# Kernel tuning notes

Hardware: AMD Instinct MI355X
Metric: run time of the kernel (lower is better)

## Reference

```python
import jax, jax.numpy as jnp
import numpy as np

D_MODEL, D_K, D_V, N_HEADS = 1024, 64, 64, 16
BATCH, N_CTX = 2, 2048


def half_causal_allowed(n):
    # rows [0, n/2): attend to cols [0, n/2) only (dense block)
    # rows [n/2, n): standard causal (col <= row)
    i = jnp.arange(n)[:, None]
    j = jnp.arange(n)[None, :]
    top = (i < n // 2) & (j < n // 2)
    bot = (i >= n // 2) & (j <= i)
    return top | bot  # [n, n] bool


def setup_inputs() -> dict:
    key = jax.random.key(0)
    ks = jax.random.split(key, 8)
    s_in = 1.0 / np.sqrt(D_MODEL)
    s_out = 1.0 / np.sqrt(D_V * N_HEADS)
    return {
        "x": jax.random.normal(ks[0], (BATCH, N_CTX, D_MODEL), jnp.float32),
        # Linear weights stored [in, out] (transpose of torch layout)
        "Wq": jax.random.uniform(ks[1], (D_MODEL, D_K * N_HEADS), jnp.float32, -s_in, s_in),
        "bq": jax.random.uniform(ks[2], (D_K * N_HEADS,), jnp.float32, -s_in, s_in),
        "Wk": jax.random.uniform(ks[3], (D_MODEL, D_K * N_HEADS), jnp.float32, -s_in, s_in),
        "bk": jax.random.uniform(ks[4], (D_K * N_HEADS,), jnp.float32, -s_in, s_in),
        "Wv": jax.random.uniform(ks[5], (D_MODEL, D_V * N_HEADS), jnp.float32, -s_in, s_in),
        "bv": jax.random.uniform(ks[6], (D_V * N_HEADS,), jnp.float32, -s_in, s_in),
        "Wo": jax.random.uniform(ks[7], (D_V * N_HEADS, D_MODEL), jnp.float32, -s_out, s_out),
    }


def reference(x, Wq, bq, Wk, bk, Wv, bv, Wo):
    b, n, _ = x.shape
    h, dk, dv = N_HEADS, D_K, D_V
    # projections -> [b, h, n, d]
    q = (x @ Wq + bq).reshape(b, n, h, dk).transpose(0, 2, 1, 3)
    k = (x @ Wk + bk).reshape(b, n, h, dk).transpose(0, 2, 1, 3)
    v = (x @ Wv + bv).reshape(b, n, h, dv).transpose(0, 2, 1, 3)
    scores = jnp.einsum("bhqd,bhkd->bhqk", q / jnp.sqrt(jnp.float32(dk)), k)
    allowed = half_causal_allowed(n)  # [n, n]
    scores = jnp.where(allowed, scores, -jnp.inf)
    attn = jax.nn.softmax(scores, axis=-1)  # dropout p=0 -> identity
    out = jnp.einsum("bhqk,bhkd->bhqd", attn, v)
    out = out.transpose(0, 2, 1, 3).reshape(b, n, h * dv)
    return out @ Wo  # final Linear has no bias
```

## Files before the change

kernel.cpp:

```cpp
#include <hip/hip_runtime.h>
#include <hip/hip_bf16.h>

#define NH 16
#define DH 64
#define DM 1024
#define NC 2048
#define MROWS 4096
#define KVT 64

#define SCALE_Q 0.180336880f

typedef __attribute__((ext_vector_type(8))) short short8;
typedef __attribute__((ext_vector_type(4))) float f32x4;
typedef __attribute__((ext_vector_type(16))) float f32x16;
typedef __attribute__((ext_vector_type(4))) unsigned int uint4e;

__device__ __forceinline__ unsigned pkbf16(float a, float b) {
    unsigned r;
    asm("v_cvt_pk_bf16_f32 %0, %1, %2" : "=v"(r) : "v"(a), "v"(b));
    return r;
}
__device__ __forceinline__ unsigned short f2bf(float x) {
    return (unsigned short)(pkbf16(x, x) & 0xffffu);
}
__device__ __forceinline__ float exp2v(float x) {
    float r;
    asm("v_exp_f32 %0, %1" : "=v"(r) : "v"(x));
    return r;
}
__device__ __forceinline__ f32x16 fzero16() {
    f32x16 r;
    #pragma unroll
    for (int i = 0; i < 16; ++i) r[i] = 0.f;
    return r;
}
__device__ __forceinline__ short8 mk8(unsigned w0, unsigned w1, unsigned w2, unsigned w3) {
    uint4e u = {w0, w1, w2, w3};
    return __builtin_bit_cast(short8, u);
}
__device__ __forceinline__ void gload16(const unsigned short* g, unsigned short* l) {
    __builtin_amdgcn_global_load_lds(
        (const __attribute__((address_space(1))) void*)g,
        (__attribute__((address_space(3))) void*)l, 16, 0, 0);
}

__global__ __launch_bounds__(256) void prep(const float* __restrict__ x,
                                            const float* __restrict__ W0,
                                            const float* __restrict__ W1,
                                            const float* __restrict__ W2,
                                            const float* __restrict__ W3,
                                            unsigned short* __restrict__ xb,
                                            unsigned short* __restrict__ Wt4)
{
    __shared__ unsigned short T[64][72];
    const int bid = blockIdx.x;
    const int t = threadIdx.x;
    if (bid < 1024) {
        #pragma unroll
        for (int g = 0; g < 2; ++g) {
            const int i = bid * 512 + g * 256 + t;
            const float4 a = ((const float4*)x)[i * 2];
            const float4 b = ((const float4*)x)[i * 2 + 1];
            uint4e u = {pkbf16(a.x, a.y), pkbf16(a.z, a.w),
                        pkbf16(b.x, b.y), pkbf16(b.z, b.w)};
            ((uint4e*)xb)[i] = u;
        }
        return;
    }
    const int z = (bid - 1024) >> 8;
    const int tile = (bid - 1024) & 255;
    const int bi = tile >> 4, bj = tile & 15;
    const float* W = (z == 0) ? W0 : (z == 1) ? W1 : (z == 2) ? W2 : W3;
    unsigned short* Wt = Wt4 + (size_t)z * DM * DM;
    const int r = t >> 2, s = t & 3;
    const float* src = W + (size_t)(bi * 64 + r) * DM + bj * 64 + s * 16;
    float4 f0 = ((const float4*)src)[0];
    float4 f1 = ((const float4*)src)[1];
    float4 f2 = ((const float4*)src)[2];
    float4 f3 = ((const float4*)src)[3];
    uint2 u;
    u.x = pkbf16(f0.x, f0.y); u.y = pkbf16(f0.z, f0.w); *(uint2*)&T[r][s * 16]      = u;
    u.x = pkbf16(f1.x, f1.y); u.y = pkbf16(f1.z, f1.w); *(uint2*)&T[r][s * 16 + 4]  = u;
    u.x = pkbf16(f2.x, f2.y); u.y = pkbf16(f2.z, f2.w); *(uint2*)&T[r][s * 16 + 8]  = u;
    u.x = pkbf16(f3.x, f3.y); u.y = pkbf16(f3.z, f3.w); *(uint2*)&T[r][s * 16 + 12] = u;
    __syncthreads();
    unsigned short vals[16];
    #pragma unroll
    for (int j = 0; j < 16; ++j) vals[j] = T[s * 16 + j][r];
    unsigned short* dst = Wt + (size_t)(bj * 64 + r) * DM + bi * 64 + s * 16;
    *(short8*)(dst)     = *(short8*)&vals[0];
    *(short8*)(dst + 8) = *(short8*)&vals[8];
}

__global__ __launch_bounds__(256) void gemm_qkv(const unsigned short* __restrict__ A,
                                                const unsigned short* __restrict__ Bt,
                                                const float* __restrict__ bq,
                                                const float* __restrict__ bk,
                                                const float* __restrict__ bv,
                                                unsigned short* __restrict__ Out)
{
    __shared__ unsigned short As[128 * 32];
    __shared__ unsigned short Bs[128 * 32];
    const int t  = threadIdx.x;
    const int w  = t >> 6, l = t & 63;
    const int wr = w >> 1, wc = w & 1;
    const int m0 = blockIdx.y << 7;
    const int n0 = blockIdx.x << 7;

    f32x4 acc[4][4] = {};
    const int nkt = DM >> 5;
    for (int kt = 0; kt < nkt; ++kt) {
        #pragma unroll
        for (int j = 0; j < 2; ++j) {
            const int c0 = j * 256 + w * 64;
            const int cc = c0 + l;
            const int row = cc >> 2, qq = cc & 3;
            gload16(A  + (size_t)(m0 + row) * DM + kt * 32 + qq * 8, &As[c0 * 8]);
            gload16(Bt + (size_t)(n0 + row) * DM + kt * 32 + qq * 8, &Bs[c0 * 8]);
        }
        __syncthreads();
        short8 af[4], bf_[4];
        #pragma unroll
        for (int mi = 0; mi < 4; ++mi)
            af[mi] = *(short8*)&As[(wr * 64 + mi * 16 + (l & 15)) * 32 + (l >> 4) * 8];
        #pragma unroll
        for (int ni = 0; ni < 4; ++ni)
            bf_[ni] = *(short8*)&Bs[(wc * 64 + ni * 16 + (l & 15)) * 32 + (l >> 4) * 8];
        #pragma unroll
        for (int mi = 0; mi < 4; ++mi)
            #pragma unroll
            for (int ni = 0; ni < 4; ++ni)
                acc[mi][ni] = __builtin_amdgcn_mfma_f32_16x16x32_bf16(
                                  af[mi], bf_[ni], acc[mi][ni], 0, 0, 0);
        __syncthreads();
    }

    const int seg = n0 >> 10;
    const float* bias = (seg == 0) ? bq : (seg == 1) ? bk : bv;
    const float scale = (seg == 0) ? SCALE_Q : 1.0f;
    const int ncol0 = (n0 & 1023) + wc * 64;
    float bvv[4];
    #pragma unroll
    for (int ni = 0; ni < 4; ++ni)
        bvv[ni] = bias[ncol0 + ni * 16 + (l & 15)];

    if (seg == 2) {
        unsigned short* vt = Out + 2 * (size_t)MROWS * DM;
        #pragma unroll
        for (int mi = 0; mi < 4; ++mi)
            #pragma unroll
            for (int ni = 0; ni < 4; ++ni) {
                const int gcol = ncol0 + ni * 16 + (l & 15);
                const int h_ = gcol >> 6, d_ = gcol & 63;
                #pragma unroll
                for (int r = 0; r < 4; ++r) {
                    const int grow = m0 + wr * 64 + mi * 16 + (l >> 4) * 4 + r;
                    const int b_ = grow >> 11, n_ = grow & 2047;
                    vt[(((size_t)b_ * 16 + h_) * 64 + d_) * NC + n_] =
                        f2bf(acc[mi][ni][r] + bvv[ni]);
                }
            }
    } else {
        unsigned short* C = Out + (size_t)seg * MROWS * DM;
        #pragma unroll
        for (int mi = 0; mi < 4; ++mi)
            #pragma unroll
            for (int ni = 0; ni < 4; ++ni) {
                const int gcol = ncol0 + ni * 16 + (l & 15);
                #pragma unroll
                for (int r = 0; r < 4; ++r) {
                    const int grow = m0 + wr * 64 + mi * 16 + (l >> 4) * 4 + r;
                    C[(size_t)grow * DM + gcol] = f2bf((acc[mi][ni][r] + bvv[ni]) * scale);
                }
            }
    }
}

__global__ __launch_bounds__(256) void gemm_wo(const unsigned short* __restrict__ A,
                                               const unsigned short* __restrict__ Bt,
                                               float* __restrict__ C)
{
    __shared__ unsigned short As[64 * 32];
    __shared__ unsigned short Bs[128 * 32];
    const int t = threadIdx.x, w = t >> 6, l = t & 63;
    const int wr = w >> 1, wc = w & 1;
    const int m0 = blockIdx.y << 6;
    const int n0 = blockIdx.x << 7;

    f32x4 acc[2][4] = {};
    const int nkt = DM >> 5;
    for (int kt = 0; kt < nkt; ++kt) {
        {
            const int c0 = w * 64;
            const int cc = c0 + l;
            const int row = cc >> 2, qq = cc & 3;
            gload16(A + (size_t)(m0 + row) * DM + kt * 32 + qq * 8, &As[c0 * 8]);
        }
        #pragma unroll
        for (int j = 0; j < 2; ++j) {
            const int c0 = j * 256 + w * 64;
            const int cc = c0 + l;
            const int row = cc >> 2, qq = cc & 3;
            gload16(Bt + (size_t)(n0 + row) * DM + kt * 32 + qq * 8, &Bs[c0 * 8]);
        }
        __syncthreads();
        short8 af[2], bf_[4];
        #pragma unroll
        for (int mi = 0; mi < 2; ++mi)
            af[mi] = *(short8*)&As[(wr * 32 + mi * 16 + (l & 15)) * 32 + (l >> 4) * 8];
        #pragma unroll
        for (int ni = 0; ni < 4; ++ni)
            bf_[ni] = *(short8*)&Bs[(wc * 64 + ni * 16 + (l & 15)) * 32 + (l >> 4) * 8];
        #pragma unroll
        for (int mi = 0; mi < 2; ++mi)
            #pragma unroll
            for (int ni = 0; ni < 4; ++ni)
                acc[mi][ni] = __builtin_amdgcn_mfma_f32_16x16x32_bf16(
                                  af[mi], bf_[ni], acc[mi][ni], 0, 0, 0);
        __syncthreads();
    }
    #pragma unroll
    for (int mi = 0; mi < 2; ++mi)
        #pragma unroll
        for (int ni = 0; ni < 4; ++ni) {
            const int gcol = n0 + wc * 64 + ni * 16 + (l & 15);
            #pragma unroll
            for (int r = 0; r < 4; ++r) {
                const int grow = m0 + wr * 32 + mi * 16 + (l >> 4) * 4 + r;
                C[(size_t)grow * DM + gcol] = acc[mi][ni][r];
            }
        }
}

__global__ __launch_bounds__(128, 2) void attn_nosm(const unsigned short* __restrict__ Qg,
                                                    const unsigned short* __restrict__ Kg,
                                                    const unsigned short* __restrict__ Vtg,
                                                    unsigned short* __restrict__ Og)
{
    __shared__ unsigned short KS[2][4096];
    __shared__ unsigned short VS[2][4096];
    const int t   = threadIdx.x;
    const int w   = t >> 6;
    const int l   = t & 63;
    const int l31 = l & 31;
    const int hi  = l >> 5;

    const int f   = blockIdx.x;
    const int xcd = f & 7;
    const int pos = f >> 3;
    const int bh  = xcd * 4 + (pos >> 5);
    int qt = pos & 31;
    if ((pos >> 5) & 1) qt = 31 - qt;
    const int b = bh >> 4;
    const int h = bh & 15;

    const int qb = qt << 6;
    const int wq = qb + w * 32;
    const size_t rb0 = (size_t)b * NC;
    const int hd = h * DH;

    const unsigned short* qp = Qg + (rb0 + wq + l31) * DM + hd + hi * 8;
    short8 fq[4];
    #pragma unroll
    for (int c = 0; c < 4; ++c)
        fq[c] = *(const short8*)(qp + c * 16);

    f32x16 o0 = fzero16(), o1 = fzero16();
    f32x16 lacc = fzero16();
    const bool bottom = (qb >= NC / 2);
    const int nkv = bottom ? (qt + 1) : 16;

    const unsigned short* Vbase = Vtg + (size_t)bh * 64 * NC;

    auto stage = [&](int it, int buf) {
        const int kb = it * KVT;
        #pragma unroll
        for (int j = 0; j < 4; ++j) {
            const int jj  = w * 4 + j;
            const int p   = jj * 64 + l;
            const int row = p >> 3;
            const int slot = (p & 7) ^ (row & 7);
            gload16(Kg + (size_t)(rb0 + kb + row) * DM + hd + slot * 8,
                    &KS[buf][jj * 512]);
            gload16(Vbase + (size_t)row * NC + kb + slot * 8,
                    &VS[buf][jj * 512]);
        }
    };

    stage(0, 0);
    if (nkv > 1) stage(1, 1);

    for (int it = 0; it < nkv; ++it) {
        const int kb = it * KVT;
        const int cur = it & 1;
        if (it + 1 < nkv) {
            asm volatile("s_waitcnt vmcnt(8)" ::: "memory");
        } else {
            asm volatile("s_waitcnt vmcnt(0)" ::: "memory");
        }
        __builtin_amdgcn_s_barrier();

        short8 kf[2][4], vf[2][4];
        #pragma unroll
        for (int half = 0; half < 2; ++half) {
            const int row = half * 32 + l31;
            const int rx  = row & 7;
            #pragma unroll
            for (int c = 0; c < 4; ++c) {
                const int slot = (c * 2 + hi) ^ rx;
                kf[half][c] = *(const short8*)(&KS[cur][row * 64 + slot * 8]);
                vf[half][c] = *(const short8*)(&VS[cur][row * 64 + slot * 8]);
            }
        }
        asm volatile("s_waitcnt lgkmcnt(0)" ::: "memory");
        __builtin_amdgcn_sched_barrier(0);
        __builtin_amdgcn_s_barrier();

        if (it + 2 < nkv) stage(it + 2, cur);

        const bool active = bottom ? (kb <= wq + 31) : true;
        if (active) {
            f32x16 s0 = fzero16(), s1 = fzero16();
            __builtin_amdgcn_s_setprio(1);
            #pragma unroll
            for (int c = 0; c < 4; ++c) {
                s0 = __builtin_amdgcn_mfma_f32_32x32x16_bf16(kf[0][c], fq[c], s0, 0, 0, 0);
                s1 = __builtin_amdgcn_mfma_f32_32x32x16_bf16(kf[1][c], fq[c], s1, 0, 0, 0);
            }
            __builtin_amdgcn_s_setprio(0);
            if (bottom && (kb + KVT - 1 > wq)) {
                const int qg = wq + l31;
                #pragma unroll
                for (int r = 0; r < 16; ++r) {
                    const int kk = (r & 3) + 8 * (r >> 2) + 4 * hi;
                    if (kb + kk > qg)      s0[r] = -1e30f;
                    if (kb + 32 + kk > qg) s1[r] = -1e30f;
                }
            }
            #pragma unroll
            for (int r = 0; r < 16; ++r) s0[r] = exp2v(s0[r]);
            #pragma unroll
            for (int r = 0; r < 16; ++r) s1[r] = exp2v(s1[r]);
            #pragma unroll
            for (int r = 0; r < 16; ++r) lacc[r] += s0[r] + s1[r];
            __builtin_amdgcn_s_setprio(1);
            #pragma unroll
            for (int kc = 0; kc < 4; ++kc) {
                const f32x16 src = (kc < 2) ? s0 : s1;
                const int rbase = (kc & 1) * 8;
                unsigned A01 = pkbf16(src[rbase + 0], src[rbase + 1]);
                unsigned A23 = pkbf16(src[rbase + 2], src[rbase + 3]);
                unsigned A45 = pkbf16(src[rbase + 4], src[rbase + 5]);
                unsigned A67 = pkbf16(src[rbase + 6], src[rbase + 7]);
                unsigned s01 = (unsigned)__shfl_xor((int)A01, 32);
                unsigned s23 = (unsigned)__shfl_xor((int)A23, 32);
                unsigned s45 = (unsigned)__shfl_xor((int)A45, 32);
                unsigned s67 = (unsigned)__shfl_xor((int)A67, 32);
                short8 fp = hi ? mk8(s45, s67, A45, A67)
                               : mk8(A01, A23, s01, s23);
                o0 = __builtin_amdgcn_mfma_f32_32x32x16_bf16(vf[0][kc], fp, o0, 0, 0, 0);
                o1 = __builtin_amdgcn_mfma_f32_32x32x16_bf16(vf[1][kc], fp, o1, 0, 0, 0);
            }
            __builtin_amdgcn_s_setprio(0);
        }
    }
    __syncthreads();

    float lr[8];
    #pragma unroll
    for (int r = 0; r < 8; ++r) lr[r] = lacc[r] + lacc[r + 8];
    #pragma unroll
    for (int st = 4; st > 0; st >>= 1)
        #pragma unroll
        for (int r = 0; r < 4; ++r)
            if (r < st) lr[r] += lr[r + st];
    const float lrun = lr[0] + __shfl_xor(lr[0], 32);
    const float inv = 1.f / lrun;

    unsigned short* obuf = (unsigned short*)&KS[0][0];
    {
        unsigned short* reg = obuf + (size_t)(w * 32 + l31) * 72;
        #pragma unroll
        for (int r = 0; r < 16; ++r) {
            const int dd = (r & 3) + 8 * (r >> 2) + 4 * hi;
            reg[dd]      = f2bf(o0[r] * inv);
            reg[dd + 32] = f2bf(o1[r] * inv);
        }
    }
    __syncthreads();
    {
        const int row = t >> 1, seg = t & 1;
        const unsigned short* src = obuf + (size_t)row * 72 + seg * 32;
        unsigned short* dst = Og + (rb0 + qb + row) * DM + hd + seg * 32;
        #pragma unroll
        for (int i = 0; i < 4; ++i)
            *(short8*)(dst + i * 8) = *(const short8*)(src + i * 8);
    }
}

extern "C" void kernel_launch(void* const* d_in, const int* in_sizes, int n_in,
                              void* d_out, int out_size, void* d_ws, size_t ws_size,
                              hipStream_t stream)
{
    const float* x  = (const float*)d_in[0];
    const float* Wq = (const float*)d_in[1];
    const float* bq = (const float*)d_in[2];
    const float* Wk = (const float*)d_in[3];
    const float* bk = (const float*)d_in[4];
    const float* Wv = (const float*)d_in[5];
    const float* bv = (const float*)d_in[6];
    const float* Wo = (const float*)d_in[7];
    float* out = (float*)d_out;

    char* ws = (char*)d_ws;
    const size_t szA = (size_t)MROWS * DM * 2;
    const size_t szW = (size_t)DM * DM * 2;
    unsigned short* xb  = (unsigned short*)(ws);
    unsigned short* wqT = (unsigned short*)(ws + szA);
    unsigned short* woT = (unsigned short*)(ws + szA + 3 * szW);
    unsigned short* qb_ = (unsigned short*)(ws + szA + 4 * szW);
    unsigned short* kb_ = (unsigned short*)(ws + 2 * szA + 4 * szW);
    unsigned short* vt_ = (unsigned short*)(ws + 3 * szA + 4 * szW);
    unsigned short* ab_ = (unsigned short*)(ws + 4 * szA + 4 * szW);

    prep<<<dim3(2048), 256, 0, stream>>>(x, Wq, Wk, Wv, Wo, xb, wqT);
    gemm_qkv<<<dim3(24, 32), 256, 0, stream>>>(xb, wqT, bq, bk, bv, qb_);
    attn_nosm<<<dim3(1024), 128, 0, stream>>>(qb_, kb_, vt_, ab_);
    gemm_wo<<<dim3(8, 64), 256, 0, stream>>>(ab_, woT, out);
}
```

Before: 112.1 us.

## Store V in MFMA-fragment layout, load it straight to registers, use 128-wide KV tiles

The QKV GEMM epilogue now writes V in a pre-swizzled, fragment-ready layout. The attention kernel can then load V operands straight from global memory into registers instead of staging them through LDS. The KV tile grows from 64 to 128 keys: K shares a doubled LDS buffer, and each iteration processes two 64-key sub-tiles. This halves the loop trip count and barrier count, and removes V's LDS traffic. In exchange, global-load latency for V is exposed inside the loop, the per-warp skip of fully masked blocks is gone, and some wholly masked work is computed on the diagonal tile.

```diff
diff --git a/kernel.cpp b/kernel.cpp
--- a/kernel.cpp
+++ b/kernel.cpp
@@ -6,7 +6,6 @@
 #define DM 1024
 #define NC 2048
 #define MROWS 4096
-#define KVT 64
 
 #define SCALE_Q 0.180336880f
 
@@ -145,7 +144,7 @@
         bvv[ni] = bias[ncol0 + ni * 16 + (l & 15)];
 
     if (seg == 2) {
-        unsigned short* vt = Out + 2 * (size_t)MROWS * DM;
+        unsigned short* vf = Out + 2 * (size_t)MROWS * DM;
         #pragma unroll
         for (int mi = 0; mi < 4; ++mi)
             #pragma unroll
@@ -155,9 +154,13 @@
                 #pragma unroll
                 for (int r = 0; r < 4; ++r) {
                     const int grow = m0 + wr * 64 + mi * 16 + (l >> 4) * 4 + r;
-                    const int b_ = grow >> 11, n_ = grow & 2047;
-                    vt[(((size_t)b_ * 16 + h_) * 64 + d_) * NC + n_] =
-                        f2bf(acc[mi][ni][r] + bvv[ni]);
+                    const int n  = grow & 2047;
+                    const int bh = (grow >> 11) * 16 + h_;
+                    const int tt = n >> 6, nl = n & 63;
+                    const int kc = nl >> 4, h2 = (nl >> 3) & 1, e = nl & 7;
+                    const int half = d_ >> 5;
+                    vf[((((size_t)bh * 32 + tt) * 2 + half) * 4 + kc) * 512 +
+                       ((d_ & 31) + 32 * h2) * 8 + e] = f2bf(acc[mi][ni][r] + bvv[ni]);
                 }
             }
     } else {
@@ -232,13 +235,12 @@
         }
 }
 
-__global__ __launch_bounds__(128, 2) void attn_nosm(const unsigned short* __restrict__ Qg,
-                                                    const unsigned short* __restrict__ Kg,
-                                                    const unsigned short* __restrict__ Vtg,
-                                                    unsigned short* __restrict__ Og)
+__global__ __launch_bounds__(128, 2) void attn128(const unsigned short* __restrict__ Qg,
+                                                  const unsigned short* __restrict__ Kg,
+                                                  const unsigned short* __restrict__ Vfg,
+                                                  unsigned short* __restrict__ Og)
 {
-    __shared__ unsigned short KS[2][4096];
-    __shared__ unsigned short VS[2][4096];
+    __shared__ unsigned short KS[2][8192];
     const int t   = threadIdx.x;
     const int w   = t >> 6;
     const int l   = t & 63;
@@ -268,22 +270,20 @@
     f32x16 o0 = fzero16(), o1 = fzero16();
     f32x16 lacc = fzero16();
     const bool bottom = (qb >= NC / 2);
-    const int nkv = bottom ? (qt + 1) : 16;
-
-    const unsigned short* Vbase = Vtg + (size_t)bh * 64 * NC;
+    const int nkv = bottom ? ((qt >> 1) + 1) : 8;
+
+    const unsigned short* Vbase = Vfg + (size_t)bh * 64 * NC + l * 8;
 
     auto stage = [&](int it, int buf) {
-        const int kb = it * KVT;
-        #pragma unroll
-        for (int j = 0; j < 4; ++j) {
-            const int jj  = w * 4 + j;
+        const int kb = it * 128;
+        #pragma unroll
+        for (int j = 0; j < 8; ++j) {
+            const int jj  = w * 8 + j;
             const int p   = jj * 64 + l;
             const int row = p >> 3;
             const int slot = (p & 7) ^ (row & 7);
             gload16(Kg + (size_t)(rb0 + kb + row) * DM + hd + slot * 8,
                     &KS[buf][jj * 512]);
-            gload16(Vbase + (size_t)row * NC + kb + slot * 8,
-                    &VS[buf][jj * 512]);
         }
     };
 
@@ -291,7 +291,6 @@
     if (nkv > 1) stage(1, 1);
 
     for (int it = 0; it < nkv; ++it) {
-        const int kb = it * KVT;
         const int cur = it & 1;
         if (it + 1 < nkv) {
             asm volatile("s_waitcnt vmcnt(8)" ::: "memory");
@@ -300,35 +299,53 @@
         }
         __builtin_amdgcn_s_barrier();
 
-        short8 kf[2][4], vf[2][4];
-        #pragma unroll
-        for (int half = 0; half < 2; ++half) {
-            const int row = half * 32 + l31;
+        short8 kf[4][4];
+        #pragma unroll
+        for (int q4 = 0; q4 < 4; ++q4) {
+            const int row = q4 * 32 + l31;
             const int rx  = row & 7;
             #pragma unroll
             for (int c = 0; c < 4; ++c) {
                 const int slot = (c * 2 + hi) ^ rx;
-                kf[half][c] = *(const short8*)(&KS[cur][row * 64 + slot * 8]);
-                vf[half][c] = *(const short8*)(&VS[cur][row * 64 + slot * 8]);
+                kf[q4][c] = *(const short8*)(&KS[cur][row * 64 + slot * 8]);
             }
         }
         asm volatile("s_waitcnt lgkmcnt(0)" ::: "memory");
         __builtin_amdgcn_sched_barrier(0);
         __builtin_amdgcn_s_barrier();
 
+        short8 vA[8], vB[8];
+        {
+            const int t0 = it * 2;
+            #pragma unroll
+            for (int half = 0; half < 2; ++half)
+                #pragma unroll
+                for (int kc = 0; kc < 4; ++kc)
+                    vA[half * 4 + kc] = *(const short8*)
+                        (Vbase + (((size_t)(t0) * 2 + half) * 4 + kc) * 512);
+            #pragma unroll
+            for (int half = 0; half < 2; ++half)
+                #pragma unroll
+                for (int kc = 0; kc < 4; ++kc)
+                    vB[half * 4 + kc] = *(const short8*)
+                        (Vbase + (((size_t)(t0 + 1) * 2 + half) * 4 + kc) * 512);
+        }
         if (it + 2 < nkv) stage(it + 2, cur);
 
-        const bool active = bottom ? (kb <= wq + 31) : true;
-        if (active) {
+        const bool lastTile = (it == nkv - 1);
+        #pragma unroll
+        for (int hh = 0; hh < 2; ++hh) {
+            const int kb = it * 128 + hh * 64;
+            const short8* vf = hh ? vB : vA;
             f32x16 s0 = fzero16(), s1 = fzero16();
             __builtin_amdgcn_s_setprio(1);
             #pragma unroll
             for (int c = 0; c < 4; ++c) {
-                s0 = __builtin_amdgcn_mfma_f32_32x32x16_bf16(kf[0][c], fq[c], s0, 0, 0, 0);
-                s1 = __builtin_amdgcn_mfma_f32_32x32x16_bf16(kf[1][c], fq[c], s1, 0, 0, 0);
+                s0 = __builtin_amdgcn_mfma_f32_32x32x16_bf16(kf[hh*2][c],   fq[c], s0, 0, 0, 0);
+                s1 = __builtin_amdgcn_mfma_f32_32x32x16_bf16(kf[hh*2+1][c], fq[c], s1, 0, 0, 0);
             }
             __builtin_amdgcn_s_setprio(0);
-            if (bottom && (kb + KVT - 1 > wq)) {
+            if (bottom && lastTile) {
                 const int qg = wq + l31;
                 #pragma unroll
                 for (int r = 0; r < 16; ++r) {
@@ -358,8 +375,8 @@
                 unsigned s67 = (unsigned)__shfl_xor((int)A67, 32);
                 short8 fp = hi ? mk8(s45, s67, A45, A67)
                                : mk8(A01, A23, s01, s23);
-                o0 = __builtin_amdgcn_mfma_f32_32x32x16_bf16(vf[0][kc], fp, o0, 0, 0, 0);
-                o1 = __builtin_amdgcn_mfma_f32_32x32x16_bf16(vf[1][kc], fp, o1, 0, 0, 0);
+                o0 = __builtin_amdgcn_mfma_f32_32x32x16_bf16(vf[kc],     fp, o0, 0, 0, 0);
+                o1 = __builtin_amdgcn_mfma_f32_32x32x16_bf16(vf[4 + kc], fp, o1, 0, 0, 0);
             }
             __builtin_amdgcn_s_setprio(0);
         }
@@ -420,11 +437,11 @@
     unsigned short* woT = (unsigned short*)(ws + szA + 3 * szW);
     unsigned short* qb_ = (unsigned short*)(ws + szA + 4 * szW);
     unsigned short* kb_ = (unsigned short*)(ws + 2 * szA + 4 * szW);
-    unsigned short* vt_ = (unsigned short*)(ws + 3 * szA + 4 * szW);
+    unsigned short* vf_ = (unsigned short*)(ws + 3 * szA + 4 * szW);
     unsigned short* ab_ = (unsigned short*)(ws + 4 * szA + 4 * szW);
 
     prep<<<dim3(2048), 256, 0, stream>>>(x, Wq, Wk, Wv, Wo, xb, wqT);
     gemm_qkv<<<dim3(24, 32), 256, 0, stream>>>(xb, wqT, bq, bk, bv, qb_);
-    attn_nosm<<<dim3(1024), 128, 0, stream>>>(qb_, kb_, vt_, ab_);
+    attn128<<<dim3(1024), 128, 0, stream>>>(qb_, kb_, vf_, ab_);
     gemm_wo<<<dim3(8, 64), 256, 0, stream>>>(ab_, woT, out);
 }
```

Result: slower. 149.3 us (+33.1%).
